# Performance work log

Hardware: AMD Instinct MI355X
Metric: run time of the kernel (lower is better)

Reference implementation:

```python
import jax, jax.numpy as jnp
import numpy as np

TAU = 2.0      # tau_thr in the source
EPS = 1e-5     # BatchNorm1d default eps
ALPHA = 8.0    # ATan surrogate alpha


@jax.custom_vjp
def atan_spike(x):
    # Heaviside forward, ATan surrogate backward (spikingjelly surrogate.ATan)
    return (x >= 0.0).astype(x.dtype)

def _as_fwd(x):
    return atan_spike(x), x

def _as_bwd(x, g):
    sg = (ALPHA / 2.0) / (1.0 + (jnp.pi / 2.0 * ALPHA * x) ** 2)
    return (g * sg,)

atan_spike.defvjp(_as_fwd, _as_bwd)


def lif(x, thr=1.0):
    # Multi-step LIFNode: v <- v + (x - v)/tau ; spike = H(v - thr);
    # hard reset to v_reset=0 with detach_reset=True.
    def step(v, xt):
        v = v + (xt - v) / TAU
        s = atan_spike(v - thr)
        v = v * (1.0 - jax.lax.stop_gradient(s))
        return v, s
    _, s = jax.lax.scan(step, jnp.zeros_like(x[0]), x)
    return s


def bn(x, p):
    # inference BatchNorm1d over channel dim C of [T,B,C,N]; p = [gamma,beta,mean,var] each [C]
    g, b, m, v = p
    inv = g / jnp.sqrt(v + EPS)
    return x * inv[:, None] + (b - m * inv)[:, None]


def setup_inputs() -> dict:
    key = jax.random.key(0)
    ks = jax.random.split(key, 11)
    T, B, C, H, W = 4, 64, 384, 14, 14
    sc = C ** -0.5
    x = jax.random.normal(ks[0], (T, B, C, H, W), jnp.float32)
    q_w = jax.random.normal(ks[1], (C, C), jnp.float32) * sc
    k_w = jax.random.normal(ks[2], (C, C), jnp.float32) * sc
    v_w = jax.random.normal(ks[3], (C, C), jnp.float32) * sc
    proj_w = jax.random.normal(ks[4], (C, C), jnp.float32) * sc
    proj_b = jax.random.normal(ks[5], (C,), jnp.float32) * 0.02
    def bn_params(k):
        return jax.random.uniform(k, (4, C), jnp.float32, 0.1, 1.0)
    return {
        'x': x, 'q_w': q_w, 'k_w': k_w, 'v_w': v_w,
        'proj_w': proj_w, 'proj_b': proj_b,
        'q_bn_p': bn_params(ks[6]), 'k_bn_p': bn_params(ks[7]),
        'v_bn_p': bn_params(ks[8]), 'p_bn_p': bn_params(ks[9]),
    }


def reference(x, q_w, k_w, v_w, proj_w, proj_b, q_bn_p, k_bn_p, v_bn_p, p_bn_p):
    T, B, C, H, W = x.shape
    nh = 8
    d = C // nh
    N = H * W
    identity = x

    xs = lif(x).reshape(T, B, C, N)  # binary spikes [T,B,C,N]

    def branch(w, p):
        # conv1x1 (C->C) + BN + LIF, then split heads -> [T,B,h,N,d]
        y = bn(jnp.einsum('tbcn,dc->tbdn', xs, w), p)
        s = lif(y)
        return s.reshape(T, B, nh, d, N).transpose(0, 1, 2, 4, 3)

    q = branch(q_w, q_bn_p)
    k = branch(k_w, k_bn_p)
    v = branch(v_w, v_bn_p)

    # unnormalized binary attention (no softmax)
    attn = jnp.einsum('tbhnd,tbhmd->tbhnm', q, k)      # [T,B,h,N,N]
    y = jnp.einsum('tbhnm,tbhmd->tbhnd', attn, v) * 0.125

    y = y.transpose(0, 1, 2, 4, 3).reshape(T, B, C, N)  # merge heads back to C
    y = lif(y, thr=0.5)                                 # attn_lif, v_threshold=0.5

    y = jnp.einsum('tbcn,dc->tbdn', y, proj_w) + proj_b[:, None]
    y = bn(y, p_bn_p)
    return y.reshape(T, B, C, H, W) + identity
```

## Files before the change

### kernel.cpp

```cpp
#include <hip/hip_runtime.h>
#include <hip/hip_bf16.h>

typedef unsigned short u16;
typedef unsigned char  u8;
typedef unsigned int   u32;
typedef __attribute__((ext_vector_type(8))) short  short8;
typedef __attribute__((ext_vector_type(8))) __bf16 bf16x8;
typedef __attribute__((ext_vector_type(4))) float  f32x4;
typedef __attribute__((ext_vector_type(4))) int    i32x4;

#define DI static __device__ __forceinline__

constexpr int T_ = 4, B_ = 64, C_ = 384, N_ = 196, NH_ = 8, DH_ = 48;
constexpr int J1_ = B_ * N_;
constexpr int J_  = T_ * J1_;
constexpr int K2_ = 2 * C_;
constexpr int M1_ = 3 * C_;

DI u16 f2bf(float x){ __hip_bfloat16 h = __float2bfloat16(x); u16 u; __builtin_memcpy(&u,&h,2); return u; }
DI float bf2f(u16 u){ __hip_bfloat16 h; __builtin_memcpy(&h,&u,2); return __bfloat162float(h); }

DI void gload16(const void* g, void* lds){
  __builtin_amdgcn_global_load_lds((const __attribute__((address_space(1))) u32*)g,
                                   (__attribute__((address_space(3))) u32*)lds, 16, 0, 0);
}
DI bf16x8 ldbf8(const u16* p){ short8 v = *(const short8*)p; return __builtin_bit_cast(bf16x8, v); }
DI int SWZ(int n){ return ((n >> 3) ^ (n >> 5)) & 3; }

__global__ __launch_bounds__(256) void k0_prep(
    const float* __restrict__ qw, const float* __restrict__ kw,
    const float* __restrict__ vw, const float* __restrict__ pw,
    const float* __restrict__ qbn, const float* __restrict__ kbn,
    const float* __restrict__ vbn, const float* __restrict__ pbn,
    u16* __restrict__ A2f, u16* __restrict__ A2pf,
    float* __restrict__ invq, float* __restrict__ betaq,
    float* __restrict__ invp, float* __restrict__ betap)
{
  int id = blockIdx.x * 256 + threadIdx.x;
  const int nAf = M1_ * K2_;
  const int nPf = C_ * K2_;
  if (id < nAf) {
    int tmp = id;
    int e    = tmp & 7;  tmp >>= 3;
    int lane = tmp & 63; tmp >>= 6;
    int ks2  = tmp & 1;  tmp >>= 1;
    int mt   = tmp & 3;  tmp >>= 2;
    int wm   = tmp & 1;  tmp >>= 1;
    int kt   = tmp % 12;
    int bm   = tmp / 12;
    int cc = bm*128 + wm*64 + mt*16 + (lane & 15);
    int k  = kt*64 + ks2*32 + (lane >> 4)*8 + e;
    int br = cc / C_, row = cc % C_;
    const float* w = (br == 0) ? qw : ((br == 1) ? kw : vw);
    float wv = w[row * C_ + (k < C_ ? k : k - C_)];
    u16 hi = f2bf(wv);
    A2f[id] = (k < C_) ? hi : f2bf(__fsub_rn(wv, bf2f(hi)));
  } else if (id < nAf + nPf) {
    int tmp = id - nAf;
    int id2 = tmp;
    int e    = tmp & 7;  tmp >>= 3;
    int lane = tmp & 63; tmp >>= 6;
    int ks2  = tmp & 1;  tmp >>= 1;
    int mt   = tmp & 3;  tmp >>= 2;
    int wm   = tmp & 1;  tmp >>= 1;
    int kt   = tmp % 12;
    int bm   = tmp / 12;
    int cc = bm*128 + wm*64 + mt*16 + (lane & 15);
    int k  = kt*64 + ks2*32 + (lane >> 4)*8 + e;
    float wv = pw[cc * C_ + (k < C_ ? k : k - C_)];
    u16 hi = f2bf(wv);
    A2pf[id2] = (k < C_) ? hi : f2bf(__fsub_rn(wv, bf2f(hi)));
  } else if (id < nAf + nPf + M1_) {
    int c = id - nAf - nPf;
    int br = c / C_, cr = c % C_;
    const float* p = (br == 0) ? qbn : ((br == 1) ? kbn : vbn);
    float g = p[cr], bb = p[C_ + cr], mm = p[2*C_ + cr], vv = p[3*C_ + cr];
    float inv = g / sqrtf(__fadd_rn(vv, 1e-5f));
    invq[c] = inv; betaq[c] = __fsub_rn(bb, __fmul_rn(mm, inv));
  } else if (id < nAf + nPf + M1_ + C_) {
    int c = id - nAf - nPf - M1_;
    float g = pbn[c], bb = pbn[C_ + c], mm = pbn[2*C_ + c], vv = pbn[3*C_ + c];
    float inv = g / sqrtf(__fadd_rn(vv, 1e-5f));
    invp[c] = inv; betap[c] = __fsub_rn(bb, __fmul_rn(mm, inv));
  }
}

__global__ __launch_bounds__(256) void k1_lif_x(const float* __restrict__ x, u16* __restrict__ xs_t)
{
  int b = blockIdx.x / 12, ch = blockIdx.x % 12;
  int c0 = ch * 32;
  __shared__ u16 sp[4 * 32 * 198];
  int tid = threadIdx.x;
  for (int idx = tid; idx < 32 * N_; idx += 256) {
    int ci = idx / N_, n = idx % N_;
    float v = 0.f;
    for (int t = 0; t < 4; t++) {
      float xv = x[((size_t)((t*B_ + b)*C_ + c0 + ci))*N_ + n];
      v = __fadd_rn(v, __fmul_rn(__fsub_rn(xv, v), 0.5f));
      bool s = (v >= 1.0f);
      sp[(t*32 + ci)*198 + n] = s ? (u16)0x3F80 : (u16)0;
      v = __fmul_rn(v, s ? 0.f : 1.f);
    }
  }
  __syncthreads();
  for (int idx = tid; idx < 4 * 32 * N_; idx += 256) {
    int ci = idx & 31; int q = idx >> 5; int n = q % N_; int t = q / N_;
    xs_t[((size_t)((t*B_ + b)*N_ + n))*C_ + c0 + ci] = sp[(t*32 + ci)*198 + n];
  }
}

__global__ __launch_bounds__(256, 2) void g1_branch(
    const u16* __restrict__ A2f, const u16* __restrict__ xs_t,
    const float* __restrict__ invq, const float* __restrict__ betaq,
    u8* __restrict__ qs, u8* __restrict__ ks_, u8* __restrict__ vs)
{
  int blk = blockIdx.x;
  int grp = blk / 72, rem = blk % 72;
  int bm = rem >> 3;
  int jt = grp * 8 + (rem & 7);
  if (jt >= 98) return;
  int cc0 = bm * 128;
  int colb = jt * 128;

  __shared__ u16 Bt[128 * 64];

  int tid = threadIdx.x;
  int lane = tid & 63, w = tid >> 6;
  int lr = lane & 15, lg = lane >> 4;
  int rsw = lr & 7;
  int wm = w & 1;
  int mrow = wm * 64, ncol = (w >> 1) * 64;

  float vst[4][4][4];
  #pragma unroll
  for (int a = 0; a < 4; a++)
    #pragma unroll
    for (int bq = 0; bq < 4; bq++)
      #pragma unroll
      for (int r = 0; r < 4; r++) vst[a][bq][r] = 0.f;

  f32x4 acc[4][4];
  bf16x8 af[2][4];

  auto LOADA = [&](int kt2) {
    int wb = (bm * 12 + kt2) * 2 + wm;
    #pragma unroll
    for (int ks2 = 0; ks2 < 2; ks2++)
      #pragma unroll
      for (int mt = 0; mt < 4; mt++)
        af[ks2][mt] = ldbf8(A2f + ((size_t)(((wb * 4 + mt) * 2 + ks2) * 64) + lane) * 8);
  };

  LOADA(0);

  for (int u = 0; u < 48; u++) {
    int t = u / 12, kt = u - t * 12;
    int ckB0 = kt * 64;
    int ckB = (ckB0 >= C_) ? (ckB0 - C_) : ckB0;
    long j0 = (long)t * J1_ + colb;

    #pragma unroll
    for (int i = 0; i < 4; i++) {
      int L0 = tid + i * 256;
      int r = L0 >> 3;
      int c = (L0 & 7) ^ (r & 7);
      gload16(xs_t + (size_t)(j0 + r) * C_ + ckB + c * 8, &Bt[L0 * 8]);
    }

    if (kt == 0) {
      #pragma unroll
      for (int a = 0; a < 4; a++)
        #pragma unroll
        for (int bq = 0; bq < 4; bq++) acc[a][bq] = (f32x4){0.f, 0.f, 0.f, 0.f};
    }
    __syncthreads();

    #pragma unroll
    for (int ks2 = 0; ks2 < 2; ks2++) {
      bf16x8 bfr[4];
      #pragma unroll
      for (int nn = 0; nn < 4; nn++)
        bfr[nn] = ldbf8(&Bt[(ncol + nn*16 + lr)*64 + (((ks2*4 + lg) ^ rsw) * 8)]);
      #pragma unroll
      for (int mt = 0; mt < 4; mt++)
        #pragma unroll
        for (int nn = 0; nn < 4; nn++)
          acc[mt][nn] = __builtin_amdgcn_mfma_f32_16x16x32_bf16(af[ks2][mt], bfr[nn], acc[mt][nn], 0, 0, 0);
    }

    if (u + 1 < 48) {
      int un = u + 1;
      LOADA(un - (un / 12) * 12);
    }

    if (kt == 11) {
      #pragma unroll
      for (int mt = 0; mt < 4; mt++) {
        #pragma unroll
        for (int r = 0; r < 4; r++) {
          int cc = cc0 + mrow + mt*16 + lg*4 + r;
          float inv = invq[cc], beta = betaq[cc];
          int br = cc / C_, c = cc % C_;
          u8* dst = ((br == 0) ? qs : ((br == 1) ? ks_ : vs)) + (size_t)c * J_ + t * J1_ + colb;
          #pragma unroll
          for (int nn = 0; nn < 4; nn++) {
            int col = ncol + nn*16 + lr;
            float yb = __fadd_rn(__fmul_rn(acc[mt][nn][r], inv), beta);
            float v = vst[mt][nn][r];
            v = __fadd_rn(v, __fmul_rn(__fsub_rn(yb, v), 0.5f));
            bool sgl = (v >= 1.0f);
            vst[mt][nn][r] = __fmul_rn(v, sgl ? 0.f : 1.f);
            dst[col] = sgl ? (u8)1 : (u8)0;
          }
        }
      }
    }
    __syncthreads();
  }
}

__global__ __launch_bounds__(256) void k3_attn(
    const u8* __restrict__ qs, const u8* __restrict__ ks_, const u8* __restrict__ vs,
    u16* __restrict__ s2t)
{
  int b = blockIdx.x >> 3, h = blockIdx.x & 7;
  __shared__ __align__(16) signed char qL[208 * 80];
  __shared__ __align__(16) signed char kL[208 * 80];
  __shared__ __align__(16) signed char vL[48 * 272];
  __shared__ __align__(16) signed char aL[4 * 16 * 272];

  int tid = threadIdx.x, lane = tid & 63, w = tid >> 6;
  int lr = lane & 15, lg = lane >> 4;

  for (int i = tid; i < 208*80/4; i += 256) { ((int*)qL)[i] = 0; ((int*)kL)[i] = 0; }
  for (int i = tid; i < 48*272/4; i += 256) ((int*)vL)[i] = 0;
  for (int i = tid; i < 4*16*272/4; i += 256) ((int*)aL)[i] = 0;
  __syncthreads();

  float vst[4][3][4];
  #pragma unroll
  for (int a = 0; a < 4; a++)
    #pragma unroll
    for (int d = 0; d < 3; d++)
      #pragma unroll
      for (int r = 0; r < 4; r++) vst[a][d][r] = 0.f;

  signed char* arow = &aL[w * 16 * 272];
  const i32x4 zero4 = {0, 0, 0, 0};

  for (int t = 0; t < 4; t++) {
    size_t off = (size_t)(t*B_ + b) * N_;
    for (int i = tid; i < 588; i += 256) {
      int dd4 = i / 49, n4 = i - dd4 * 49;
      size_t rb = (size_t)(h*DH_ + dd4*4) * J_ + off + n4*4;
      u32 q0 = *(const u32*)(qs + rb);
      u32 q1 = *(const u32*)(qs + rb + J_);
      u32 q2 = *(const u32*)(qs + rb + 2*(size_t)J_);
      u32 q3 = *(const u32*)(qs + rb + 3*(size_t)J_);
      u32 k0 = *(const u32*)(ks_ + rb);
      u32 k1 = *(const u32*)(ks_ + rb + J_);
      u32 k2 = *(const u32*)(ks_ + rb + 2*(size_t)J_);
      u32 k3 = *(const u32*)(ks_ + rb + 3*(size_t)J_);
      u32 v0 = *(const u32*)(vs + rb);
      u32 v1 = *(const u32*)(vs + rb + J_);
      u32 v2 = *(const u32*)(vs + rb + 2*(size_t)J_);
      u32 v3 = *(const u32*)(vs + rb + 3*(size_t)J_);
      int c16 = dd4 >> 2, bb4 = (dd4 & 3) << 2;
      #pragma unroll
      for (int jj = 0; jj < 4; jj++) {
        u32 tq = ((q0 >> (8*jj)) & 0xFFu) | (((q1 >> (8*jj)) & 0xFFu) << 8)
               | (((q2 >> (8*jj)) & 0xFFu) << 16) | (((q3 >> (8*jj)) & 0xFFu) << 24);
        u32 tk = ((k0 >> (8*jj)) & 0xFFu) | (((k1 >> (8*jj)) & 0xFFu) << 8)
               | (((k2 >> (8*jj)) & 0xFFu) << 16) | (((k3 >> (8*jj)) & 0xFFu) << 24);
        int n = n4*4 + jj;
        int cs = ((c16 ^ SWZ(n)) << 4) + bb4;
        *(u32*)(qL + n*80 + cs) = tq;
        *(u32*)(kL + n*80 + cs) = tk;
      }
      *(u32*)(vL + (dd4*4 + 0)*272 + n4*4) = v0;
      *(u32*)(vL + (dd4*4 + 1)*272 + n4*4) = v1;
      *(u32*)(vL + (dd4*4 + 2)*272 + n4*4) = v2;
      *(u32*)(vL + (dd4*4 + 3)*272 + n4*4) = v3;
    }
    __syncthreads();

    int nslots = (w == 0) ? 4 : 3;
    for (int sl = 0; sl < nslots; sl++) {
      int ni = w + sl * 4;
      int nq = ni*16 + lr;
      i32x4 bq = *reinterpret_cast<const i32x4*>(qL + nq*80 + ((lg ^ SWZ(nq)) << 4));
      for (int mj = 0; mj < 13; mj++) {
        int mk = mj*16 + lr;
        i32x4 ak = *reinterpret_cast<const i32x4*>(kL + mk*80 + ((lg ^ SWZ(mk)) << 4));
        i32x4 d = __builtin_amdgcn_mfma_i32_16x16x64_i8(ak, bq, zero4, 0, 0, 0);
        u32 pk = (u32)d[0] | ((u32)d[1] << 8) | ((u32)d[2] << 16) | ((u32)d[3] << 24);
        *(u32*)(arow + lr*272 + mj*16 + lg*4) = pk;
      }
      #pragma unroll
      for (int di = 0; di < 3; di++) {
        i32x4 acc = zero4;
        #pragma unroll
        for (int ks2 = 0; ks2 < 4; ks2++) {
          i32x4 aa = *reinterpret_cast<const i32x4*>(arow + lr*272 + ks2*64 + lg*16);
          i32x4 bb = *reinterpret_cast<const i32x4*>(vL + (di*16 + lr)*272 + ks2*64 + lg*16);
          acc = __builtin_amdgcn_mfma_i32_16x16x64_i8(aa, bb, acc, 0, 0, 0);
        }
        #pragma unroll
        for (int r = 0; r < 4; r++) {
          int n = ni*16 + lg*4 + r;
          float xv = __fmul_rn((float)acc[r], 0.125f);
          float v = vst[sl][di][r];
          v = __fadd_rn(v, __fmul_rn(__fsub_rn(xv, v), 0.5f));
          bool s = (v >= 0.5f);
          vst[sl][di][r] = __fmul_rn(v, s ? 0.f : 1.f);
          if (n < N_)
            s2t[((size_t)((t*B_ + b)*N_ + n))*C_ + h*DH_ + di*16 + lr] = s ? (u16)0x3F80 : (u16)0;
        }
      }
    }
    __syncthreads();
  }
}

__global__ __launch_bounds__(256, 2) void g2_proj(
    const u16* __restrict__ A2pf, const u16* __restrict__ s2t,
    const float* __restrict__ invp, const float* __restrict__ betap,
    const float* __restrict__ pb, const float* __restrict__ x,
    float* __restrict__ out)
{
  int blk = blockIdx.x;
  int grp = blk / 24, rem = blk % 24;
  int bm = rem >> 3;
  int bn = grp * 8 + (rem & 7);
  int cc0 = bm * 128, j0 = bn * 128;

  __shared__ u16 Bt[128 * 64];

  int tid = threadIdx.x;
  int lane = tid & 63, w = tid >> 6;
  int lr = lane & 15, lg = lane >> 4;
  int rsw = lr & 7;
  int wm = w & 1;
  int mrow = wm * 64, ncol = (w >> 1) * 64;

  f32x4 acc[4][4];
  #pragma unroll
  for (int a = 0; a < 4; a++)
    #pragma unroll
    for (int bq = 0; bq < 4; bq++) acc[a][bq] = (f32x4){0.f, 0.f, 0.f, 0.f};

  bf16x8 af[2][4];
  auto LOADA = [&](int kt2) {
    int wb = (bm * 12 + kt2) * 2 + wm;
    #pragma unroll
    for (int ks2 = 0; ks2 < 2; ks2++)
      #pragma unroll
      for (int mt = 0; mt < 4; mt++)
        af[ks2][mt] = ldbf8(A2pf + ((size_t)(((wb * 4 + mt) * 2 + ks2) * 64) + lane) * 8);
  };

  LOADA(0);

  for (int kt = 0; kt < 12; kt++) {
    int ckB0 = kt * 64;
    int ckB = (ckB0 >= C_) ? (ckB0 - C_) : ckB0;
    #pragma unroll
    for (int i = 0; i < 4; i++) {
      int L0 = tid + i * 256;
      int r = L0 >> 3;
      int c = (L0 & 7) ^ (r & 7);
      gload16(s2t + (size_t)(j0 + r) * C_ + ckB + c * 8, &Bt[L0 * 8]);
    }
    __syncthreads();

    #pragma unroll
    for (int ks2 = 0; ks2 < 2; ks2++) {
      bf16x8 bfr[4];
      #pragma unroll
      for (int nn = 0; nn < 4; nn++)
        bfr[nn] = ldbf8(&Bt[(ncol + nn*16 + lr)*64 + (((ks2*4 + lg) ^ rsw) * 8)]);
      #pragma unroll
      for (int mt = 0; mt < 4; mt++)
        #pragma unroll
        for (int nn = 0; nn < 4; nn++)
          acc[mt][nn] = __builtin_amdgcn_mfma_f32_16x16x32_bf16(af[ks2][mt], bfr[nn], acc[mt][nn], 0, 0, 0);
    }

    if (kt < 11) LOADA(kt + 1);
    __syncthreads();
  }

  #pragma unroll
  for (int mt = 0; mt < 4; mt++) {
    #pragma unroll
    for (int r = 0; r < 4; r++) {
      int cc = cc0 + mrow + mt*16 + lg*4 + r;
      float inv = invp[cc], beta = betap[cc], pbv = pb[cc];
      #pragma unroll
      for (int nn = 0; nn < 4; nn++) {
        int j = j0 + ncol + nn*16 + lr;
        float y = __fadd_rn(acc[mt][nn][r], pbv);
        float o = __fadd_rn(__fmul_rn(y, inv), beta);
        int jq = j / N_, n = j % N_;
        size_t addr = ((size_t)jq * C_ + cc) * N_ + n;
        out[addr] = __fadd_rn(o, x[addr]);
      }
    }
  }
}

extern "C" void kernel_launch(void* const* d_in, const int* in_sizes, int n_in,
                              void* d_out, int out_size, void* d_ws, size_t ws_size,
                              hipStream_t stream)
{
  (void)in_sizes; (void)n_in; (void)out_size; (void)ws_size;
  const float* x   = (const float*)d_in[0];
  const float* qw  = (const float*)d_in[1];
  const float* kw  = (const float*)d_in[2];
  const float* vw  = (const float*)d_in[3];
  const float* pw  = (const float*)d_in[4];
  const float* pbv = (const float*)d_in[5];
  const float* qbn = (const float*)d_in[6];
  const float* kbn = (const float*)d_in[7];
  const float* vbn = (const float*)d_in[8];
  const float* pbn = (const float*)d_in[9];

  char* ws = (char*)d_ws;
  u16*   A2f   = (u16*)  (ws + 0);
  u16*   A2pf  = (u16*)  (ws + 1769472);
  float* invq  = (float*)(ws + 2359296);
  float* betaq = (float*)(ws + 2363904);
  float* invp  = (float*)(ws + 2368512);
  float* betap = (float*)(ws + 2370048);
  u16*   xs_t  = (u16*)  (ws + 2371584);
  u16*   s2t   = xs_t;
  u8*    qs    = (u8*)   (ws + 40906752);
  u8*    ks    = (u8*)   (ws + 60174336);
  u8*    vs    = (u8*)   (ws + 79441920);

  k0_prep<<<4614, 256, 0, stream>>>(qw, kw, vw, pw, qbn, kbn, vbn, pbn,
                                    A2f, A2pf, invq, betaq, invp, betap);
  k1_lif_x<<<768, 256, 0, stream>>>(x, xs_t);
  g1_branch<<<936, 256, 0, stream>>>(A2f, xs_t, invq, betaq, qs, ks, vs);
  k3_attn<<<512, 256, 0, stream>>>(qs, ks, vs, s2t);
  g2_proj<<<1176, 256, 0, stream>>>(A2pf, s2t, invp, betap, pbv, x, (float*)d_out);
}
```

Measured before the change: 300.0 us.

## Double-buffer B tiles in LDS for branch and projection GEMMs

Result: no change. 302.5 us (+0.8%).

```diff
diff --git a/kernel.cpp b/kernel.cpp
--- a/kernel.cpp
+++ b/kernel.cpp
@@ -122,7 +122,7 @@
   int cc0 = bm * 128;
   int colb = jt * 128;
 
-  __shared__ u16 Bt[128 * 64];
+  __shared__ u16 Bt[2][128 * 64];
 
   int tid = threadIdx.x;
   int lane = tid & 63, w = tid >> 6;
@@ -142,30 +142,39 @@
   f32x4 acc[4][4];
   bf16x8 af[2][4];
 
-  auto LOADA = [&](int kt2) {
-    int wb = (bm * 12 + kt2) * 2 + wm;
-    #pragma unroll
-    for (int ks2 = 0; ks2 < 2; ks2++)
-      #pragma unroll
-      for (int mt = 0; mt < 4; mt++)
-        af[ks2][mt] = ldbf8(A2f + ((size_t)(((wb * 4 + mt) * 2 + ks2) * 64) + lane) * 8);
-  };
-
-  LOADA(0);
-
-  for (int u = 0; u < 48; u++) {
-    int t = u / 12, kt = u - t * 12;
-    int ckB0 = kt * 64;
-    int ckB = (ckB0 >= C_) ? (ckB0 - C_) : ckB0;
-    long j0 = (long)t * J1_ + colb;
-
+  auto STAGE = [&](int bi, int u2) {
+    int t2 = u2 / 12, kt2 = u2 % 12;
+    long j0 = (long)t2 * J1_ + colb;
+    int ck0 = kt2 * 64;
+    int ckB = (ck0 >= C_) ? (ck0 - C_) : ck0;
     #pragma unroll
     for (int i = 0; i < 4; i++) {
       int L0 = tid + i * 256;
       int r = L0 >> 3;
       int c = (L0 & 7) ^ (r & 7);
-      gload16(xs_t + (size_t)(j0 + r) * C_ + ckB + c * 8, &Bt[L0 * 8]);
-    }
+      gload16(xs_t + (size_t)(j0 + r) * C_ + ckB + c * 8, &Bt[bi][L0 * 8]);
+    }
+  };
+
+  auto LOADA = [&](int kt2) {
+    int wb = (bm * 12 + kt2) * 2 + wm;
+    #pragma unroll
+    for (int ks2 = 0; ks2 < 2; ks2++)
+      #pragma unroll
+      for (int mt = 0; mt < 4; mt++)
+        af[ks2][mt] = ldbf8(A2f + ((size_t)(((wb * 4 + mt) * 2 + ks2) * 64) + lane) * 8);
+  };
+
+  STAGE(0, 0);
+  LOADA(0);
+  asm volatile("s_waitcnt vmcnt(0)" ::: "memory");
+  __builtin_amdgcn_s_barrier();
+
+  for (int u = 0; u < 48; u++) {
+    int t = u / 12, kt = u - t * 12;
+    int cur = u & 1;
+
+    if (u + 1 < 48) STAGE(cur ^ 1, u + 1);
 
     if (kt == 0) {
       #pragma unroll
@@ -173,14 +182,13 @@
         #pragma unroll
         for (int bq = 0; bq < 4; bq++) acc[a][bq] = (f32x4){0.f, 0.f, 0.f, 0.f};
     }
-    __syncthreads();
 
     #pragma unroll
     for (int ks2 = 0; ks2 < 2; ks2++) {
       bf16x8 bfr[4];
       #pragma unroll
       for (int nn = 0; nn < 4; nn++)
-        bfr[nn] = ldbf8(&Bt[(ncol + nn*16 + lr)*64 + (((ks2*4 + lg) ^ rsw) * 8)]);
+        bfr[nn] = ldbf8(&Bt[cur][(ncol + nn*16 + lr)*64 + (((ks2*4 + lg) ^ rsw) * 8)]);
       #pragma unroll
       for (int mt = 0; mt < 4; mt++)
         #pragma unroll
@@ -215,7 +223,12 @@
         }
       }
     }
-    __syncthreads();
+
+    if (u < 47) {
+      if (kt == 11) asm volatile("s_waitcnt vmcnt(0)" ::: "memory");
+      else          asm volatile("s_waitcnt vmcnt(8)" ::: "memory");
+      __builtin_amdgcn_s_barrier();
+    }
   }
 }
 
@@ -334,7 +347,7 @@
   int bn = grp * 8 + (rem & 7);
   int cc0 = bm * 128, j0 = bn * 128;
 
-  __shared__ u16 Bt[128 * 64];
+  __shared__ u16 Bt[2][128 * 64];
 
   int tid = threadIdx.x;
   int lane = tid & 63, w = tid >> 6;
@@ -350,35 +363,42 @@
     for (int bq = 0; bq < 4; bq++) acc[a][bq] = (f32x4){0.f, 0.f, 0.f, 0.f};
 
   bf16x8 af[2][4];
-  auto LOADA = [&](int kt2) {
-    int wb = (bm * 12 + kt2) * 2 + wm;
-    #pragma unroll
-    for (int ks2 = 0; ks2 < 2; ks2++)
-      #pragma unroll
-      for (int mt = 0; mt < 4; mt++)
-        af[ks2][mt] = ldbf8(A2pf + ((size_t)(((wb * 4 + mt) * 2 + ks2) * 64) + lane) * 8);
-  };
-
-  LOADA(0);
-
-  for (int kt = 0; kt < 12; kt++) {
-    int ckB0 = kt * 64;
-    int ckB = (ckB0 >= C_) ? (ckB0 - C_) : ckB0;
+
+  auto STAGE = [&](int bi, int kt2) {
+    int ck0 = kt2 * 64;
+    int ckB = (ck0 >= C_) ? (ck0 - C_) : ck0;
     #pragma unroll
     for (int i = 0; i < 4; i++) {
       int L0 = tid + i * 256;
       int r = L0 >> 3;
       int c = (L0 & 7) ^ (r & 7);
-      gload16(s2t + (size_t)(j0 + r) * C_ + ckB + c * 8, &Bt[L0 * 8]);
-    }
-    __syncthreads();
+      gload16(s2t + (size_t)(j0 + r) * C_ + ckB + c * 8, &Bt[bi][L0 * 8]);
+    }
+  };
+  auto LOADA = [&](int kt2) {
+    int wb = (bm * 12 + kt2) * 2 + wm;
+    #pragma unroll
+    for (int ks2 = 0; ks2 < 2; ks2++)
+      #pragma unroll
+      for (int mt = 0; mt < 4; mt++)
+        af[ks2][mt] = ldbf8(A2pf + ((size_t)(((wb * 4 + mt) * 2 + ks2) * 64) + lane) * 8);
+  };
+
+  STAGE(0, 0);
+  LOADA(0);
+  asm volatile("s_waitcnt vmcnt(0)" ::: "memory");
+  __builtin_amdgcn_s_barrier();
+
+  for (int kt = 0; kt < 12; kt++) {
+    int cur = kt & 1;
+    if (kt + 1 < 12) STAGE(cur ^ 1, kt + 1);
 
     #pragma unroll
     for (int ks2 = 0; ks2 < 2; ks2++) {
       bf16x8 bfr[4];
       #pragma unroll
       for (int nn = 0; nn < 4; nn++)
-        bfr[nn] = ldbf8(&Bt[(ncol + nn*16 + lr)*64 + (((ks2*4 + lg) ^ rsw) * 8)]);
+        bfr[nn] = ldbf8(&Bt[cur][(ncol + nn*16 + lr)*64 + (((ks2*4 + lg) ^ rsw) * 8)]);
       #pragma unroll
       for (int mt = 0; mt < 4; mt++)
         #pragma unroll
@@ -386,8 +406,11 @@
           acc[mt][nn] = __builtin_amdgcn_mfma_f32_16x16x32_bf16(af[ks2][mt], bfr[nn], acc[mt][nn], 0, 0, 0);
     }
 
-    if (kt < 11) LOADA(kt + 1);
-    __syncthreads();
+    if (kt + 1 < 12) {
+      LOADA(kt + 1);
+      asm volatile("s_waitcnt vmcnt(8)" ::: "memory");
+      __builtin_amdgcn_s_barrier();
+    }
   }
 
   #pragma unroll
```
